# Kernel optimization log

Hardware: AMD Instinct MI355X
Metric: run time of the kernel (lower is better)

## Reference

```python
import jax, jax.numpy as jnp
import numpy as np

EPS = 1e-12  # F.normalize default eps (denominator = max(norm, eps))


def setup_inputs() -> dict:
    key = jax.random.key(0)
    ks = jax.random.split(key, 8)
    B, FIN, H, W = 4, 256, 64, 64
    N_MEM, SQ = 64, 16           # sqrt_fin = fin**0.5
    POS_CH = 2                    # PosEncoding concatenates one coord channel per dim
    CIN = FIN + POS_CH
    QK = N_MEM * SQ               # 1024
    # PosEncoding buffer: normalized coordinate grid in [-1, 1], shape [2, H, W]
    ys = jnp.linspace(-1.0, 1.0, H, dtype=jnp.float32)
    xs = jnp.linspace(-1.0, 1.0, W, dtype=jnp.float32)
    gy, gx = jnp.meshgrid(ys, xs, indexing='ij')
    pos = jnp.stack([gy, gx], axis=0)
    s = 0.02
    return {
        'x':    jax.random.normal(ks[0], (B, FIN, H, W), jnp.float32),
        'pos':  pos,
        'wq':   jax.random.normal(ks[1], (QK, CIN), jnp.float32) * s,
        'bq':   jnp.zeros((QK,), jnp.float32),
        'wk':   jax.random.normal(ks[2], (QK, CIN), jnp.float32) * s,
        'bk':   jnp.zeros((QK,), jnp.float32),
        'v':    jax.random.normal(ks[3], (N_MEM, FIN), jnp.float32) * s,
        'wout': jax.random.normal(ks[4], (FIN, FIN), jnp.float32) * s,
        'bout': jnp.zeros((FIN,), jnp.float32),
    }


def reference(x, pos, wq, bq, wk, bk, v, wout, bout):
    B, C, H, W = x.shape
    S = H * W
    n_mem, fin = v.shape
    sq = wq.shape[0] // n_mem
    # PosEncoding: concat coordinate channels
    posb = jnp.broadcast_to(pos[None], (B,) + pos.shape)
    xp = jnp.concatenate([x, posb], axis=1).reshape(B, C + pos.shape[0], S)
    # 1x1 conv projections (channel GEMMs)
    q = jnp.einsum('oc,bcs->bos', wq, xp) + bq[None, :, None]  # [B, n_mem*sq, S]
    k = jnp.einsum('oc,bcs->bos', wk, xp) + bk[None, :, None]
    q = q.reshape(B, n_mem, sq, S).transpose(0, 3, 1, 2)  # [B,S,m,sq]
    k = k.reshape(B, n_mem, sq, S).transpose(0, 3, 2, 1)  # [B,S,sq,m]
    # F.normalize: q over last dim (sqrt_fin), k over dim=1 (sqrt_fin)
    qn = q / jnp.maximum(jnp.linalg.norm(q, axis=-1, keepdims=True), EPS)
    kn = k / jnp.maximum(jnp.linalg.norm(k, axis=2, keepdims=True), EPS)
    # attn[b,s,m,n] = qn . kn ; dropout is identity in eval mode.
    # mean over memory slots m commutes with (attn @ v), so fuse:
    attn_mean = jnp.einsum('bsk,bskn->bsn', qn.mean(axis=2), kn)  # [B,S,n_mem]
    mem = attn_mean @ v                                            # [B,S,fin]
    mem = mem.transpose(0, 2, 1).reshape(B, fin, H, W)
    out = jnp.einsum('of,bfhw->bohw', wout, mem) + bout[None, :, None, None]
    return x + out
```

## Files before the change

### kernel.cpp

```cpp
#include <hip/hip_runtime.h>
#include <stdint.h>

#define EPSN 1e-12f

typedef float f32x4 __attribute__((ext_vector_type(4)));
typedef __bf16 bf16x8 __attribute__((ext_vector_type(8)));
typedef uint32_t u32x4 __attribute__((ext_vector_type(4)));

__device__ __forceinline__ unsigned short f2bf(float f) {
  union { float f; unsigned int u; } v; v.f = f;
  unsigned int u = v.u + 0x7FFFu + ((v.u >> 16) & 1u);
  return (unsigned short)(u >> 16);
}

#define WQF_OFF 0
#define WKF_OFF (64 * 9 * 64 * 8)
#define WVP_OFF (2 * 64 * 9 * 64 * 8)

__global__ __launch_bounds__(256) void prep_kernel(
    const float* __restrict__ wq, const float* __restrict__ bq,
    const float* __restrict__ wk, const float* __restrict__ bk,
    const float* __restrict__ v, const float* __restrict__ wout,
    unsigned short* __restrict__ wsp) {
  if (blockIdx.x < 144) {
    int t = blockIdx.x * 256 + threadIdx.x;
    int lane = t & 63;
    int rest = t >> 6;
    int ks = rest % 9, g = rest / 9;
    int col = lane & 15, quad = lane >> 4;
    int o = g * 16 + col;
    int kb = ks * 32 + quad * 8;
    unsigned short q8[8], k8[8];
#pragma unroll
    for (int j = 0; j < 8; ++j) {
      int k = kb + j;
      float vq, vk;
      if (k < 258)       { vq = wq[o * 258 + k]; vk = wk[o * 258 + k]; }
      else if (k == 258) { vq = bq[o];           vk = bk[o]; }
      else               { vq = 0.f;             vk = 0.f; }
      q8[j] = f2bf(vq); k8[j] = f2bf(vk);
    }
    *(u32x4*)(wsp + WQF_OFF + t * 8) = *(u32x4*)q8;
    *(u32x4*)(wsp + WKF_OFF + t * 8) = *(u32x4*)k8;
  } else {
    int idx2 = (blockIdx.x - 144) * 256 + threadIdx.x;
    int fc = idx2 & 3, m = (idx2 >> 2) & 63, o = idx2 >> 8;
    const f32x4* wo = (const f32x4*)(wout + o * 256 + fc * 64);
    const f32x4* vm = (const f32x4*)(v + m * 256 + fc * 64);
    float s = 0.f;
#pragma unroll
    for (int f = 0; f < 16; ++f) {
      f32x4 a = wo[f], bvv = vm[f];
      s += a[0]*bvv[0] + a[1]*bvv[1] + a[2]*bvv[2] + a[3]*bvv[3];
    }
    s += __shfl_xor(s, 1, 64);
    s += __shfl_xor(s, 2, 64);
    if (fc == 0) wsp[WVP_OFF + o * 64 + m] = f2bf(s);
  }
}

#define KP 296
#define QS 66

__global__ __launch_bounds__(1024) void fused_kernel(
    const float* __restrict__ x, const float* __restrict__ pos,
    const unsigned short* __restrict__ wsp, const float* __restrict__ bout,
    float* __restrict__ out) {
  __shared__ __align__(16) unsigned short xp[64 * KP];
  __shared__ __align__(16) float qbarL[16 * QS];
  __shared__ __align__(16) unsigned short attnT[64 * 72];
  __shared__ float boutL[256];

  const int tid = threadIdx.x;
  const int lane = tid & 63;
  const int wid = __builtin_amdgcn_readfirstlane(tid >> 6);
  const int col = lane & 15, quad = lane >> 4;
  const int P0 = blockIdx.x * 64;
  const int b = P0 >> 12, s0 = P0 & 4095;

  uint32_t* xp32 = (uint32_t*)xp;
  for (int i = tid; i < 64 * 152; i += 1024) {
    int dc = i & 7, pp = (i >> 3) & 63, dh = i >> 9;
    int dcol = dh * 8 + dc;
    if (dcol < 148) {
      int c0 = dcol * 2;
      float v0, v1;
      if (c0 < 256) {
        v0 = x[(b * 256 + c0) * 4096 + s0 + pp];
        v1 = x[(b * 256 + c0 + 1) * 4096 + s0 + pp];
      } else if (c0 == 256) {
        v0 = pos[s0 + pp];
        v1 = pos[4096 + s0 + pp];
      } else {
        v0 = (c0 == 258) ? 1.0f : 0.0f;
        v1 = 0.0f;
      }
      xp32[pp * 148 + dcol] =
          (uint32_t)f2bf(v0) | ((uint32_t)f2bf(v1) << 16);
    }
  }
  if (tid < 256) boutL[tid] = bout[tid];
  for (int i = tid; i < 16 * QS; i += 1024) qbarL[i] = 0.f;
  __syncthreads();

  const unsigned short* aqbase = wsp + WQF_OFF + (wid * 4 * 9 * 64 + lane) * 8;
  const unsigned short* akbase = wsp + WKF_OFF + (wid * 4 * 9 * 64 + lane) * 8;

  f32x4 acc[4][4];
#pragma unroll
  for (int ot = 0; ot < 4; ++ot)
#pragma unroll
    for (int nt = 0; nt < 4; ++nt) acc[ot][nt] = (f32x4)0.f;

  {
#pragma unroll
    for (int ks = 0; ks < 9; ++ks) {
      const int kb = ks * 32;
      bf16x8 av[4], bv[4];
#pragma unroll
      for (int ot = 0; ot < 4; ++ot)
        av[ot] = *(const bf16x8*)(aqbase + (ot * 9 + ks) * 512);
#pragma unroll
      for (int nt = 0; nt < 4; ++nt)
        bv[nt] = *(const bf16x8*)(&xp[(nt * 16 + col) * KP + kb + quad * 8]);
#pragma unroll
      for (int ot = 0; ot < 4; ++ot)
#pragma unroll
        for (int nt = 0; nt < 4; ++nt)
          acc[ot][nt] = __builtin_amdgcn_mfma_f32_16x16x32_bf16(av[ot], bv[nt], acc[ot][nt], 0, 0, 0);
    }
  }

  {
    float qsum[4][4];
#pragma unroll
    for (int nt = 0; nt < 4; ++nt)
#pragma unroll
      for (int r = 0; r < 4; ++r) qsum[nt][r] = 0.f;
#pragma unroll
    for (int ot = 0; ot < 4; ++ot) {
#pragma unroll
      for (int nt = 0; nt < 4; ++nt) {
        f32x4 a = acc[ot][nt];
        float s = a[0]*a[0] + a[1]*a[1] + a[2]*a[2] + a[3]*a[3];
        s += __shfl_xor(s, 16, 64);
        s += __shfl_xor(s, 32, 64);
        float inv = 1.0f / fmaxf(sqrtf(s), EPSN);
#pragma unroll
        for (int r = 0; r < 4; ++r) qsum[nt][r] = fmaf(a[r], inv, qsum[nt][r]);
      }
    }
#pragma unroll
    for (int nt = 0; nt < 4; ++nt)
#pragma unroll
      for (int r = 0; r < 4; ++r)
        atomicAdd(&qbarL[(quad * 4 + r) * QS + nt * 16 + col], qsum[nt][r] * (1.0f / 64.0f));
  }
  __syncthreads();

#pragma unroll
  for (int ot = 0; ot < 4; ++ot)
#pragma unroll
    for (int nt = 0; nt < 4; ++nt) acc[ot][nt] = (f32x4)0.f;

  {
#pragma unroll
    for (int ks = 0; ks < 9; ++ks) {
      const int kb = ks * 32;
      bf16x8 av[4], bv[4];
#pragma unroll
      for (int ot = 0; ot < 4; ++ot)
        av[ot] = *(const bf16x8*)(akbase + (ot * 9 + ks) * 512);
#pragma unroll
      for (int nt = 0; nt < 4; ++nt)
        bv[nt] = *(const bf16x8*)(&xp[(nt * 16 + col) * KP + kb + quad * 8]);
#pragma unroll
      for (int ot = 0; ot < 4; ++ot)
#pragma unroll
        for (int nt = 0; nt < 4; ++nt)
          acc[ot][nt] = __builtin_amdgcn_mfma_f32_16x16x32_bf16(av[ot], bv[nt], acc[ot][nt], 0, 0, 0);
    }
  }

  {
    float qb[4][4];
#pragma unroll
    for (int nt = 0; nt < 4; ++nt)
#pragma unroll
      for (int r = 0; r < 4; ++r)
        qb[nt][r] = qbarL[(quad * 4 + r) * QS + nt * 16 + col];

#pragma unroll
    for (int ot = 0; ot < 4; ++ot) {
      const int m = wid * 4 + ot;
#pragma unroll
      for (int nt = 0; nt < 4; ++nt) {
        f32x4 a = acc[ot][nt];
        float s2 = a[0]*a[0] + a[1]*a[1] + a[2]*a[2] + a[3]*a[3];
        float sp = qb[nt][0]*a[0] + qb[nt][1]*a[1] + qb[nt][2]*a[2] + qb[nt][3]*a[3];
        s2 += __shfl_xor(s2, 16, 64);
        s2 += __shfl_xor(s2, 32, 64);
        sp += __shfl_xor(sp, 16, 64);
        sp += __shfl_xor(sp, 32, 64);
        float attn = sp / fmaxf(sqrtf(s2), EPSN);
        if (quad == 0) attnT[(nt * 16 + col) * 72 + m] = f2bf(attn);
      }
    }
  }
  __syncthreads();

  {
    f32x4 e[4];
#pragma unroll
    for (int nt = 0; nt < 4; ++nt) e[nt] = (f32x4)0.f;
    const unsigned short* wvb = wsp + WVP_OFF + (wid * 16 + col) * 64 + quad * 8;
#pragma unroll
    for (int ks = 0; ks < 2; ++ks) {
      bf16x8 av = *(const bf16x8*)(wvb + ks * 32);
#pragma unroll
      for (int nt = 0; nt < 4; ++nt) {
        bf16x8 bv = *(const bf16x8*)(&attnT[(nt * 16 + col) * 72 + ks * 32 + quad * 8]);
        e[nt] = __builtin_amdgcn_mfma_f32_16x16x32_bf16(av, bv, e[nt], 0, 0, 0);
      }
    }
#pragma unroll
    for (int nt = 0; nt < 4; ++nt) {
#pragma unroll
      for (int r = 0; r < 4; ++r) {
        const int o = wid * 16 + quad * 4 + r;
        const int p = nt * 16 + col;
        const int gi = (b * 256 + o) * 4096 + s0 + p;
        out[gi] = x[gi] + boutL[o] + e[nt][r];
      }
    }
  }
}

extern "C" void kernel_launch(void* const* d_in, const int* in_sizes, int n_in,
                              void* d_out, int out_size, void* d_ws, size_t ws_size,
                              hipStream_t stream) {
  const float* x    = (const float*)d_in[0];
  const float* pos  = (const float*)d_in[1];
  const float* wq   = (const float*)d_in[2];
  const float* bq   = (const float*)d_in[3];
  const float* wk   = (const float*)d_in[4];
  const float* bk   = (const float*)d_in[5];
  const float* v    = (const float*)d_in[6];
  const float* wout = (const float*)d_in[7];
  const float* bout = (const float*)d_in[8];
  float* out = (float*)d_out;
  unsigned short* wsp = (unsigned short*)d_ws;

  hipLaunchKernelGGL(prep_kernel, dim3(400), dim3(256), 0, stream,
                     wq, bq, wk, bk, v, wout, wsp);
  hipLaunchKernelGGL(fused_kernel, dim3(256), dim3(1024), 0, stream,
                     x, pos, wsp, bout, out);
}
```

Before: 140.3 us.

## Switch fused kernel to 32x32x16 MFMA with 32-pixel tiles and doubled grid

Repacks the Q/K weights in the prep kernel for the 32x32x16 bf16 MFMA layout. Each block now handles 32 pixels instead of 64, so the grid doubles to 512 blocks. Each wave computes two 32x32 tiles per projection with a single shared B operand, and the normalisation reductions move to the new accumulator layout. The goal is to fill more CUs and use fewer, larger MFMA instructions per tile. In exchange, each weight tile is reloaded from global memory by twice as many blocks, and only 8 of the 16 waves run the output GEMM.

After: 136.4 us. 1.03x faster.

```diff
diff --git a/kernel.cpp b/kernel.cpp
--- a/kernel.cpp
+++ b/kernel.cpp
@@ -3,6 +3,7 @@
 
 #define EPSN 1e-12f
 
+typedef float f32x16 __attribute__((ext_vector_type(16)));
 typedef float f32x4 __attribute__((ext_vector_type(4)));
 typedef __bf16 bf16x8 __attribute__((ext_vector_type(8)));
 typedef uint32_t u32x4 __attribute__((ext_vector_type(4)));
@@ -14,8 +15,8 @@
 }
 
 #define WQF_OFF 0
-#define WKF_OFF (64 * 9 * 64 * 8)
-#define WVP_OFF (2 * 64 * 9 * 64 * 8)
+#define WKF_OFF (32 * 18 * 64 * 8)
+#define WVP_OFF (2 * 32 * 18 * 64 * 8)
 
 __global__ __launch_bounds__(256) void prep_kernel(
     const float* __restrict__ wq, const float* __restrict__ bq,
@@ -26,10 +27,9 @@
     int t = blockIdx.x * 256 + threadIdx.x;
     int lane = t & 63;
     int rest = t >> 6;
-    int ks = rest % 9, g = rest / 9;
-    int col = lane & 15, quad = lane >> 4;
-    int o = g * 16 + col;
-    int kb = ks * 32 + quad * 8;
+    int ks = rest % 18, g = rest / 18;
+    int o = g * 32 + (lane & 31);
+    int kb = ks * 16 + (lane >> 5) * 8;
     unsigned short q8[8], k8[8];
 #pragma unroll
     for (int j = 0; j < 8; ++j) {
@@ -60,27 +60,28 @@
 }
 
 #define KP 296
-#define QS 66
-
-__global__ __launch_bounds__(1024) void fused_kernel(
+#define QSS 33
+#define AT 72
+
+__global__ __launch_bounds__(1024, 8) void fused_kernel(
     const float* __restrict__ x, const float* __restrict__ pos,
     const unsigned short* __restrict__ wsp, const float* __restrict__ bout,
     float* __restrict__ out) {
-  __shared__ __align__(16) unsigned short xp[64 * KP];
-  __shared__ __align__(16) float qbarL[16 * QS];
-  __shared__ __align__(16) unsigned short attnT[64 * 72];
+  __shared__ __align__(16) unsigned short xp[32 * KP];
+  __shared__ __align__(16) float qbarL[16 * QSS];
+  __shared__ __align__(16) unsigned short attnM[32 * AT];
   __shared__ float boutL[256];
 
   const int tid = threadIdx.x;
   const int lane = tid & 63;
   const int wid = __builtin_amdgcn_readfirstlane(tid >> 6);
-  const int col = lane & 15, quad = lane >> 4;
-  const int P0 = blockIdx.x * 64;
+  const int px = lane & 31, q2 = lane >> 5;
+  const int P0 = blockIdx.x * 32;
   const int b = P0 >> 12, s0 = P0 & 4095;
 
   uint32_t* xp32 = (uint32_t*)xp;
-  for (int i = tid; i < 64 * 152; i += 1024) {
-    int dc = i & 7, pp = (i >> 3) & 63, dh = i >> 9;
+  for (int i = tid; i < 32 * 152; i += 1024) {
+    int dc = i & 7, pp = (i >> 3) & 31, dh = i >> 8;
     int dcol = dh * 8 + dc;
     if (dcol < 148) {
       int c0 = dcol * 2;
@@ -100,138 +101,102 @@
     }
   }
   if (tid < 256) boutL[tid] = bout[tid];
-  for (int i = tid; i < 16 * QS; i += 1024) qbarL[i] = 0.f;
+  if (tid < 16 * QSS) qbarL[tid] = 0.f;
   __syncthreads();
 
-  const unsigned short* aqbase = wsp + WQF_OFF + (wid * 4 * 9 * 64 + lane) * 8;
-  const unsigned short* akbase = wsp + WKF_OFF + (wid * 4 * 9 * 64 + lane) * 8;
-
-  f32x4 acc[4][4];
-#pragma unroll
-  for (int ot = 0; ot < 4; ++ot)
-#pragma unroll
-    for (int nt = 0; nt < 4; ++nt) acc[ot][nt] = (f32x4)0.f;
+  const unsigned short* aqb = wsp + WQF_OFF + wid * 2 * 9216 + lane * 8;
+  const unsigned short* akb = wsp + WKF_OFF + wid * 2 * 9216 + lane * 8;
+  const unsigned short* xb = &xp[px * KP + q2 * 8];
+
+  f32x16 acc0 = (f32x16)0.f, acc1 = (f32x16)0.f;
+#pragma unroll
+  for (int ks = 0; ks < 18; ++ks) {
+    bf16x8 a0 = *(const bf16x8*)(aqb + ks * 512);
+    bf16x8 a1 = *(const bf16x8*)(aqb + 9216 + ks * 512);
+    bf16x8 bv = *(const bf16x8*)(xb + ks * 16);
+    acc0 = __builtin_amdgcn_mfma_f32_32x32x16_bf16(a0, bv, acc0, 0, 0, 0);
+    acc1 = __builtin_amdgcn_mfma_f32_32x32x16_bf16(a1, bv, acc1, 0, 0, 0);
+  }
 
   {
-#pragma unroll
-    for (int ks = 0; ks < 9; ++ks) {
-      const int kb = ks * 32;
-      bf16x8 av[4], bv[4];
-#pragma unroll
-      for (int ot = 0; ot < 4; ++ot)
-        av[ot] = *(const bf16x8*)(aqbase + (ot * 9 + ks) * 512);
-#pragma unroll
-      for (int nt = 0; nt < 4; ++nt)
-        bv[nt] = *(const bf16x8*)(&xp[(nt * 16 + col) * KP + kb + quad * 8]);
-#pragma unroll
-      for (int ot = 0; ot < 4; ++ot)
-#pragma unroll
-        for (int nt = 0; nt < 4; ++nt)
-          acc[ot][nt] = __builtin_amdgcn_mfma_f32_16x16x32_bf16(av[ot], bv[nt], acc[ot][nt], 0, 0, 0);
-    }
+    float qsum[8];
+#pragma unroll
+    for (int r = 0; r < 8; ++r) qsum[r] = 0.f;
+#pragma unroll
+    for (int t = 0; t < 2; ++t) {
+      const f32x16 a = t ? acc1 : acc0;
+      float s20 = 0.f, s21 = 0.f;
+#pragma unroll
+      for (int r = 0; r < 8; ++r) { s20 = fmaf(a[r], a[r], s20); s21 = fmaf(a[r + 8], a[r + 8], s21); }
+      s20 += __shfl_xor(s20, 32, 64);
+      s21 += __shfl_xor(s21, 32, 64);
+      float i0 = 1.0f / fmaxf(sqrtf(s20), EPSN);
+      float i1 = 1.0f / fmaxf(sqrtf(s21), EPSN);
+#pragma unroll
+      for (int r = 0; r < 8; ++r) qsum[r] += a[r] * i0 + a[r + 8] * i1;
+    }
+#pragma unroll
+    for (int r = 0; r < 8; ++r) {
+      int j = (r & 3) + ((r >> 2) << 3) + (q2 << 2);
+      atomicAdd(&qbarL[j * QSS + px], qsum[r] * (1.0f / 64.0f));
+    }
+  }
+  __syncthreads();
+
+  acc0 = (f32x16)0.f; acc1 = (f32x16)0.f;
+#pragma unroll
+  for (int ks = 0; ks < 18; ++ks) {
+    bf16x8 a0 = *(const bf16x8*)(akb + ks * 512);
+    bf16x8 a1 = *(const bf16x8*)(akb + 9216 + ks * 512);
+    bf16x8 bv = *(const bf16x8*)(xb + ks * 16);
+    acc0 = __builtin_amdgcn_mfma_f32_32x32x16_bf16(a0, bv, acc0, 0, 0, 0);
+    acc1 = __builtin_amdgcn_mfma_f32_32x32x16_bf16(a1, bv, acc1, 0, 0, 0);
   }
 
   {
-    float qsum[4][4];
-#pragma unroll
-    for (int nt = 0; nt < 4; ++nt)
-#pragma unroll
-      for (int r = 0; r < 4; ++r) qsum[nt][r] = 0.f;
-#pragma unroll
-    for (int ot = 0; ot < 4; ++ot) {
-#pragma unroll
-      for (int nt = 0; nt < 4; ++nt) {
-        f32x4 a = acc[ot][nt];
-        float s = a[0]*a[0] + a[1]*a[1] + a[2]*a[2] + a[3]*a[3];
-        s += __shfl_xor(s, 16, 64);
-        s += __shfl_xor(s, 32, 64);
-        float inv = 1.0f / fmaxf(sqrtf(s), EPSN);
-#pragma unroll
-        for (int r = 0; r < 4; ++r) qsum[nt][r] = fmaf(a[r], inv, qsum[nt][r]);
+    float qb[8];
+#pragma unroll
+    for (int r = 0; r < 8; ++r) {
+      int j = (r & 3) + ((r >> 2) << 3) + (q2 << 2);
+      qb[r] = qbarL[j * QSS + px];
+    }
+#pragma unroll
+    for (int t = 0; t < 2; ++t) {
+      const f32x16 a = t ? acc1 : acc0;
+      float s20 = 0.f, s21 = 0.f, sp0 = 0.f, sp1 = 0.f;
+#pragma unroll
+      for (int r = 0; r < 8; ++r) {
+        s20 = fmaf(a[r], a[r], s20);         sp0 = fmaf(qb[r], a[r], sp0);
+        s21 = fmaf(a[r + 8], a[r + 8], s21); sp1 = fmaf(qb[r], a[r + 8], sp1);
       }
-    }
-#pragma unroll
-    for (int nt = 0; nt < 4; ++nt)
-#pragma unroll
-      for (int r = 0; r < 4; ++r)
-        atomicAdd(&qbarL[(quad * 4 + r) * QS + nt * 16 + col], qsum[nt][r] * (1.0f / 64.0f));
+      s20 += __shfl_xor(s20, 32, 64);
+      s21 += __shfl_xor(s21, 32, 64);
+      sp0 += __shfl_xor(sp0, 32, 64);
+      sp1 += __shfl_xor(sp1, 32, 64);
+      if (q2 == 0) {
+        int m0 = wid * 4 + t * 2;
+        attnM[px * AT + m0]     = f2bf(sp0 / fmaxf(sqrtf(s20), EPSN));
+        attnM[px * AT + m0 + 1] = f2bf(sp1 / fmaxf(sqrtf(s21), EPSN));
+      }
+    }
   }
   __syncthreads();
 
-#pragma unroll
-  for (int ot = 0; ot < 4; ++ot)
-#pragma unroll
-    for (int nt = 0; nt < 4; ++nt) acc[ot][nt] = (f32x4)0.f;
-
-  {
-#pragma unroll
-    for (int ks = 0; ks < 9; ++ks) {
-      const int kb = ks * 32;
-      bf16x8 av[4], bv[4];
-#pragma unroll
-      for (int ot = 0; ot < 4; ++ot)
-        av[ot] = *(const bf16x8*)(akbase + (ot * 9 + ks) * 512);
-#pragma unroll
-      for (int nt = 0; nt < 4; ++nt)
-        bv[nt] = *(const bf16x8*)(&xp[(nt * 16 + col) * KP + kb + quad * 8]);
-#pragma unroll
-      for (int ot = 0; ot < 4; ++ot)
-#pragma unroll
-        for (int nt = 0; nt < 4; ++nt)
-          acc[ot][nt] = __builtin_amdgcn_mfma_f32_16x16x32_bf16(av[ot], bv[nt], acc[ot][nt], 0, 0, 0);
-    }
-  }
-
-  {
-    float qb[4][4];
-#pragma unroll
-    for (int nt = 0; nt < 4; ++nt)
-#pragma unroll
-      for (int r = 0; r < 4; ++r)
-        qb[nt][r] = qbarL[(quad * 4 + r) * QS + nt * 16 + col];
-
-#pragma unroll
-    for (int ot = 0; ot < 4; ++ot) {
-      const int m = wid * 4 + ot;
-#pragma unroll
-      for (int nt = 0; nt < 4; ++nt) {
-        f32x4 a = acc[ot][nt];
-        float s2 = a[0]*a[0] + a[1]*a[1] + a[2]*a[2] + a[3]*a[3];
-        float sp = qb[nt][0]*a[0] + qb[nt][1]*a[1] + qb[nt][2]*a[2] + qb[nt][3]*a[3];
-        s2 += __shfl_xor(s2, 16, 64);
-        s2 += __shfl_xor(s2, 32, 64);
-        sp += __shfl_xor(sp, 16, 64);
-        sp += __shfl_xor(sp, 32, 64);
-        float attn = sp / fmaxf(sqrtf(s2), EPSN);
-        if (quad == 0) attnT[(nt * 16 + col) * 72 + m] = f2bf(attn);
-      }
-    }
-  }
-  __syncthreads();
-
-  {
-    f32x4 e[4];
-#pragma unroll
-    for (int nt = 0; nt < 4; ++nt) e[nt] = (f32x4)0.f;
-    const unsigned short* wvb = wsp + WVP_OFF + (wid * 16 + col) * 64 + quad * 8;
-#pragma unroll
-    for (int ks = 0; ks < 2; ++ks) {
-      bf16x8 av = *(const bf16x8*)(wvb + ks * 32);
-#pragma unroll
-      for (int nt = 0; nt < 4; ++nt) {
-        bf16x8 bv = *(const bf16x8*)(&attnT[(nt * 16 + col) * 72 + ks * 32 + quad * 8]);
-        e[nt] = __builtin_amdgcn_mfma_f32_16x16x32_bf16(av, bv, e[nt], 0, 0, 0);
-      }
-    }
-#pragma unroll
-    for (int nt = 0; nt < 4; ++nt) {
-#pragma unroll
-      for (int r = 0; r < 4; ++r) {
-        const int o = wid * 16 + quad * 4 + r;
-        const int p = nt * 16 + col;
-        const int gi = (b * 256 + o) * 4096 + s0 + p;
-        out[gi] = x[gi] + boutL[o] + e[nt][r];
-      }
+  if (wid < 8) {
+    f32x16 e0 = (f32x16)0.f;
+    const unsigned short* wv0 = wsp + WVP_OFF + (wid * 32 + px) * 64 + q2 * 8;
+    const unsigned short* ab = &attnM[px * AT + q2 * 8];
+#pragma unroll
+    for (int ks = 0; ks < 4; ++ks) {
+      bf16x8 a0 = *(const bf16x8*)(wv0 + ks * 16);
+      bf16x8 bv = *(const bf16x8*)(ab + ks * 16);
+      e0 = __builtin_amdgcn_mfma_f32_32x32x16_bf16(a0, bv, e0, 0, 0, 0);
+    }
+#pragma unroll
+    for (int r = 0; r < 16; ++r) {
+      const int o0 = wid * 32 + (r & 3) + (((r >> 2) & 1) << 3) + (q2 << 2) + ((r >> 3) << 4);
+      const int gi0 = (b * 256 + o0) * 4096 + s0 + px;
+      out[gi0] = x[gi0] + boutL[o0] + e0[r];
     }
   }
 }
@@ -253,6 +218,6 @@
 
   hipLaunchKernelGGL(prep_kernel, dim3(400), dim3(256), 0, stream,
                      wq, bq, wk, bk, v, wout, wsp);
-  hipLaunchKernelGGL(fused_kernel, dim3(256), dim3(1024), 0, stream,
+  hipLaunchKernelGGL(fused_kernel, dim3(512), dim3(1024), 0, stream,
                      x, pos, wsp, bout, out);
 }
```
